# Kernel optimization log

Hardware: AMD Instinct MI355X
Metric: run time of the kernel (lower is better)

The kernel has to match this reference:

```python
import jax, jax.numpy as jnp
import numpy as np

HIDDEN = 1024
HEADS = 16
HEAD_DIM = HIDDEN // HEADS  # 64
LOCAL = (128, 128)
ROPE_MAX_POS = LOCAL[0] + LOCAL[1]  # 256 (local attention branch)
ROPE_BASE = 10000.0


def make_rope_cache(max_len, dim, base):
    positions = jnp.arange(max_len, dtype=jnp.float32)
    theta = 1.0 / base ** (jnp.arange(0, dim, 2, dtype=jnp.float32) / dim)
    angles = jnp.einsum('i,j->ij', positions, theta)
    return jnp.stack([jnp.cos(angles), jnp.sin(angles)], axis=-1)  # (max_len, dim//2, 2)


def apply_rope(x, cache):
    # x: (B, S, H, D); cache: (max_pos, D//2, 2)
    S = x.shape[1]
    pos = jnp.arange(S) % cache.shape[0]
    rc = cache[pos][None, :, None, :, :]  # (1, S, 1, D//2, 2)
    xr = x.reshape(*x.shape[:-1], -1, 2)
    x0, x1 = xr[..., 0], xr[..., 1]
    c, s = rc[..., 0], rc[..., 1]
    out = jnp.stack([x0 * c - x1 * s, x1 * c + x0 * s], axis=-1)
    return out.reshape(x.shape)


def sliding_window_mask(S, window, dtype):
    rel = jnp.arange(S)[:, None] - jnp.arange(S)[None, :]
    inside = (rel >= -window[0]) & (rel <= window[1])
    return jnp.where(inside, jnp.zeros((), dtype), -jnp.inf)[None, None]  # (1,1,S,S)


def setup_inputs() -> dict:
    key = jax.random.key(0)
    k1, k2, k3, k4, k5 = jax.random.split(key, 5)
    B, S = 2, 2048
    hidden_states = jax.random.normal(k1, (B, S, HIDDEN), dtype=jnp.float32)
    Wqkv_kernel = jax.random.normal(k2, (HIDDEN, 3 * HIDDEN), dtype=jnp.float32) / np.sqrt(HIDDEN)
    Wqkv_bias = jnp.zeros((3 * HIDDEN,), dtype=jnp.float32)
    Wo_kernel = jax.random.normal(k3, (HIDDEN, HIDDEN), dtype=jnp.float32) / np.sqrt(HIDDEN)
    Wo_bias = jnp.zeros((HIDDEN,), dtype=jnp.float32)
    rope_cache = make_rope_cache(ROPE_MAX_POS, HEAD_DIM, ROPE_BASE)
    return {
        'hidden_states': hidden_states,
        'Wqkv_kernel': Wqkv_kernel,
        'Wqkv_bias': Wqkv_bias,
        'Wo_kernel': Wo_kernel,
        'Wo_bias': Wo_bias,
        'rope_cache': rope_cache,
    }


def reference(hidden_states, Wqkv_kernel, Wqkv_bias, Wo_kernel, Wo_bias, rope_cache):
    B, S, _ = hidden_states.shape
    qkv = hidden_states @ Wqkv_kernel + Wqkv_bias  # (B,S,3*HIDDEN)
    qkv = qkv.reshape(B, S, 3, HEADS, HEAD_DIM)
    q = qkv[:, :, 0]  # (B,S,H,D)
    k = qkv[:, :, 1]
    v = qkv[:, :, 2]
    q = apply_rope(q, rope_cache)
    k = apply_rope(k, rope_cache)
    # to (B,H,S,D)
    q = jnp.transpose(q, (0, 2, 1, 3))
    k = jnp.transpose(k, (0, 2, 1, 3))
    v = jnp.transpose(v, (0, 2, 1, 3))
    scale = jnp.sqrt(jnp.float32(HEAD_DIM))
    scores = jnp.einsum('bhqd,bhkd->bhqk', q, k) / scale
    mask = sliding_window_mask(S, LOCAL, scores.dtype)
    probs = jax.nn.softmax(scores + mask, axis=-1)
    out = jnp.einsum('bhqk,bhkd->bqhd', probs, v).reshape(B, S, HIDDEN)
    out = out @ Wo_kernel + Wo_bias
    return out
```

## Files before the change

### kernel.cpp

```cpp
#include <hip/hip_runtime.h>
#include <hip/hip_bf16.h>

typedef __bf16 bf16x8 __attribute__((ext_vector_type(8)));
typedef __bf16 bf16x4 __attribute__((ext_vector_type(4)));
typedef float f32x4 __attribute__((ext_vector_type(4)));

#define SLEN 2048
#define NHEADS 16
#define HDIM 64

__global__ __launch_bounds__(256) void prep(const float* __restrict__ hidden,
                                            const float* __restrict__ Wqkv,
                                            const float* __restrict__ Wo,
                                            __bf16* __restrict__ A1,
                                            __bf16* __restrict__ Wt,
                                            __bf16* __restrict__ Wot) {
    int b = blockIdx.x;
    if (b < 4096) {
        int i = b * 256 + threadIdx.x;
        float4 v = reinterpret_cast<const float4*>(hidden)[i];
        bf16x4 o = { (__bf16)v.x, (__bf16)v.y, (__bf16)v.z, (__bf16)v.w };
        reinterpret_cast<bf16x4*>(A1)[i] = o;
        return;
    }
    __shared__ float tile[32][33];
    const float* W; __bf16* Dst; int N, n0, kc, bx, wn, j0, JNv;
    if (b < 7168) {
        int bb = b - 4096;
        int bx96 = bb % 96; kc = bb / 96;
        W = Wqkv; Dst = Wt; N = 3072;
        n0 = bx96 * 32;
        bx = bx96 >> 2; wn = (bx96 >> 1) & 1; j0 = (bx96 & 1) * 2; JNv = 4;
    } else {
        int bb = b - 7168;
        int bx32 = bb % 32; kc = bb / 32;
        W = Wo; Dst = Wot; N = 1024;
        n0 = bx32 * 32;
        bx = bx32 >> 1; wn = bx32 & 1; j0 = 0; JNv = 2;
    }
    int k0 = kc * 32;
    int tx = threadIdx.x & 31, ty = threadIdx.x >> 5;
    #pragma unroll
    for (int i = ty; i < 32; i += 8)
        tile[i][tx] = W[(size_t)(k0 + i) * N + n0 + tx];
    __syncthreads();
    if (threadIdx.x < 128) {
        int jh = threadIdx.x >> 6;
        int lane = threadIdx.x & 63;
        int lrow = lane & 15, quad = lane >> 4;
        bf16x8 val;
        #pragma unroll
        for (int i = 0; i < 8; i++)
            val[i] = (__bf16)tile[quad * 8 + i][jh * 16 + lrow];
        size_t idx = ((((size_t)(bx * 32 + kc) * 2 + wn) * JNv + (j0 + jh)) * 64 + lane);
        *reinterpret_cast<bf16x8*>(Dst + idx * 8) = val;
    }
}

template <int TN>
__global__ __launch_bounds__(256) void gemm_bt(const __bf16* __restrict__ A,
                                               const __bf16* __restrict__ Bfrag,
                                               const float* __restrict__ bias,
                                               float* __restrict__ Cf,
                                               __bf16* __restrict__ Cq,
                                               __bf16* __restrict__ Ck,
                                               __bf16* __restrict__ Cv,
                                               int M, int N, int K, int epi) {
    constexpr int JN = TN / 32;
    __shared__ __align__(16) __bf16 As[2][128 * 40];

    int nb = N / TN;
    int bx = blockIdx.x % nb;
    int by = blockIdx.x / nb;
    int row0 = by * 128, col0 = bx * TN;

    int tid = threadIdx.x;
    int wave = tid >> 6, lane = tid & 63;
    int quad = lane >> 4, lrow = lane & 15;
    int wm = wave >> 1, wn = wave & 1;

    int r1 = tid >> 2;
    int kk = (tid & 3) * 8;
    const __bf16* Aptr = A + (size_t)(row0 + r1) * K + kk;

    const __bf16* Bbase = Bfrag + ((size_t)(bx * 32) * 2 + wn) * JN * 512 + (size_t)lane * 8;

    f32x4 acc[4][JN];
    f32x4 zero = {0.f, 0.f, 0.f, 0.f};
    #pragma unroll
    for (int i = 0; i < 4; i++)
        #pragma unroll
        for (int j = 0; j < JN; j++) acc[i][j] = zero;

    int nkc = K >> 5;

    {
        bf16x8 a0 = *reinterpret_cast<const bf16x8*>(Aptr);
        bf16x8 a1 = *reinterpret_cast<const bf16x8*>(Aptr + (size_t)64 * K);
        *reinterpret_cast<bf16x8*>(&As[0][r1 * 40 + kk]) = a0;
        *reinterpret_cast<bf16x8*>(&As[0][(r1 + 64) * 40 + kk]) = a1;
    }
    bf16x8 bR[JN];
    #pragma unroll
    for (int j = 0; j < JN; j++)
        bR[j] = *reinterpret_cast<const bf16x8*>(Bbase + j * 512);
    __syncthreads();

    for (int kc = 0; kc < nkc; kc++) {
        int p = kc & 1;
        bool more = (kc + 1) < nkc;
        bf16x8 aN0, aN1, bN[JN];
        if (more) {
            int k0 = (kc + 1) * 32;
            aN0 = *reinterpret_cast<const bf16x8*>(Aptr + k0);
            aN1 = *reinterpret_cast<const bf16x8*>(Aptr + (size_t)64 * K + k0);
            #pragma unroll
            for (int j = 0; j < JN; j++)
                bN[j] = *reinterpret_cast<const bf16x8*>(Bbase + (size_t)(kc + 1) * JN * 1024 + j * 512);
        }

        bf16x8 af[4];
        #pragma unroll
        for (int i = 0; i < 4; i++)
            af[i] = *reinterpret_cast<const bf16x8*>(&As[p][(wm * 64 + i * 16 + lrow) * 40 + quad * 8]);
        #pragma unroll
        for (int i = 0; i < 4; i++)
            #pragma unroll
            for (int j = 0; j < JN; j++)
                acc[i][j] = __builtin_amdgcn_mfma_f32_16x16x32_bf16(af[i], bR[j], acc[i][j], 0, 0, 0);

        if (more) {
            *reinterpret_cast<bf16x8*>(&As[p ^ 1][r1 * 40 + kk]) = aN0;
            *reinterpret_cast<bf16x8*>(&As[p ^ 1][(r1 + 64) * 40 + kk]) = aN1;
            __syncthreads();
            #pragma unroll
            for (int j = 0; j < JN; j++) bR[j] = bN[j];
        }
    }

    int part = col0 >> 10;
    #pragma unroll
    for (int i = 0; i < 4; i++) {
        int rowb = row0 + wm * 64 + i * 16 + quad * 4;
        #pragma unroll
        for (int j = 0; j < JN; j++) {
            int col = col0 + wn * (TN / 2) + j * 16 + lrow;
            float bsv = bias[col];
            #pragma unroll
            for (int r = 0; r < 4; r++) {
                int row = rowb + r;
                float v = acc[i][j][r] + bsv;
                if (epi == 0) {
                    Cf[(size_t)row * N + col] = v;
                } else {
                    int h = (col >> 6) & 15;
                    int d = col & 63;
                    int b = row >> 11;
                    int s = row & 2047;
                    __bf16* dst = (part == 0) ? Cq : ((part == 1) ? Ck : Cv);
                    dst[((size_t)(b * NHEADS + h) * SLEN + s) * HDIM + d] = (__bf16)v;
                }
            }
        }
    }
}

__device__ __forceinline__ bf16x8 rope8(bf16x8 v, f32x4 a, f32x4 b) {
    bf16x8 o;
    float e, od;
    e = (float)v[0]; od = (float)v[1];
    o[0] = (__bf16)(e * a[0] - od * a[1]); o[1] = (__bf16)(od * a[0] + e * a[1]);
    e = (float)v[2]; od = (float)v[3];
    o[2] = (__bf16)(e * a[2] - od * a[3]); o[3] = (__bf16)(od * a[2] + e * a[3]);
    e = (float)v[4]; od = (float)v[5];
    o[4] = (__bf16)(e * b[0] - od * b[1]); o[5] = (__bf16)(od * b[0] + e * b[1]);
    e = (float)v[6]; od = (float)v[7];
    o[6] = (__bf16)(e * b[2] - od * b[3]); o[7] = (__bf16)(od * b[2] + e * b[3]);
    return o;
}

__global__ __launch_bounds__(256) void rope_kernel(__bf16* __restrict__ Q,
                                                   __bf16* __restrict__ K,
                                                   const float* __restrict__ rope) {
    int idx = blockIdx.x * 256 + threadIdx.x;
    int chunk = idx & 7;
    int s = (idx >> 3) & 2047;
    int bh = idx >> 14;
    size_t off = ((size_t)bh * SLEN + s) * HDIM + chunk * 8;
    int pos = s & 255;
    const float* rp = rope + (size_t)pos * 64 + chunk * 8;
    f32x4 a = *reinterpret_cast<const f32x4*>(rp);
    f32x4 b = *reinterpret_cast<const f32x4*>(rp + 4);
    bf16x8 qv = *reinterpret_cast<bf16x8*>(Q + off);
    *reinterpret_cast<bf16x8*>(Q + off) = rope8(qv, a, b);
    bf16x8 kv = *reinterpret_cast<bf16x8*>(K + off);
    *reinterpret_cast<bf16x8*>(K + off) = rope8(kv, a, b);
}

__global__ __launch_bounds__(256) void attn_kernel(const __bf16* __restrict__ Q,
                                                   const __bf16* __restrict__ K,
                                                   const __bf16* __restrict__ V,
                                                   __bf16* __restrict__ O) {
    __shared__ __align__(16) __bf16 Vt[64][328];
    __shared__ __align__(16) __bf16 Pl[4][16][80];

    int bh = blockIdx.x & 31;
    int qt = blockIdx.x >> 5;
    int q0 = qt * 64;
    int kbase0 = q0 - 128;
    const __bf16* Qbh = Q + (size_t)bh * SLEN * HDIM;
    const __bf16* Kbh = K + (size_t)bh * SLEN * HDIM;
    const __bf16* Vbh = V + (size_t)bh * SLEN * HDIM;

    int tid = threadIdx.x;
    int wave = tid >> 6, lane = tid & 63;
    int quad = lane >> 4, lrow = lane & 15;
    int wq0 = q0 + wave * 16;

    {
        int dchunk = wave * 16;
        #pragma unroll
        for (int k = 0; k < 5; k++) {
            int off = k * 64 + lane;
            int krow = kbase0 + off;
            krow = min(max(krow, 0), SLEN - 1);
            const __bf16* vp = Vbh + (size_t)krow * HDIM + dchunk;
            bf16x8 v0 = *reinterpret_cast<const bf16x8*>(vp);
            bf16x8 v1 = *reinterpret_cast<const bf16x8*>(vp + 8);
            #pragma unroll
            for (int i = 0; i < 8; i++) {
                Vt[dchunk + i][off] = v0[i];
                Vt[dchunk + 8 + i][off] = v1[i];
            }
        }
    }

    bf16x8 qb0 = *reinterpret_cast<const bf16x8*>(Qbh + (size_t)(wq0 + lrow) * HDIM + quad * 8);
    bf16x8 qb1 = *reinterpret_cast<const bf16x8*>(Qbh + (size_t)(wq0 + lrow) * HDIM + 32 + quad * 8);

    __syncthreads();

    f32x4 zero = {0.f, 0.f, 0.f, 0.f};
    f32x4 acc[4], acc_l = zero;
    #pragma unroll
    for (int t = 0; t < 4; t++) acc[t] = zero;

    bf16x8 ones = { (__bf16)1.f, (__bf16)1.f, (__bf16)1.f, (__bf16)1.f,
                    (__bf16)1.f, (__bf16)1.f, (__bf16)1.f, (__bf16)1.f };

    int cbeg = wave >> 1;
    if (q0 < 128) { int e = (128 - q0) >> 5; if (e > cbeg) cbeg = e; }
    int cend = (16 * wave + 271) >> 5;
    { int e = (2175 - q0) >> 5; if (e < cend) cend = e; }

    auto loadK = [&](int c, bf16x8 (&kf)[2][2]) {
        int kb = kbase0 + c * 32;
        #pragma unroll
        for (int sub = 0; sub < 2; sub++) {
            int kr = kb + sub * 16 + lrow;
            int krc = min(max(kr, 0), SLEN - 1);
            const __bf16* kp = Kbh + (size_t)krc * HDIM;
            kf[sub][0] = *reinterpret_cast<const bf16x8*>(kp + quad * 8);
            kf[sub][1] = *reinterpret_cast<const bf16x8*>(kp + 32 + quad * 8);
        }
    };

    auto qkExp = [&](int c, bf16x8 (&kf)[2][2], int slot) {
        int kb = kbase0 + c * 32;
        int q = wq0 + lrow;
        #pragma unroll
        for (int sub = 0; sub < 2; sub++) {
            f32x4 st = __builtin_amdgcn_mfma_f32_16x16x32_bf16(kf[sub][0], qb0, zero, 0, 0, 0);
            st = __builtin_amdgcn_mfma_f32_16x16x32_bf16(kf[sub][1], qb1, st, 0, 0, 0);
            bf16x4 pk;
            #pragma unroll
            for (int r = 0; r < 4; r++) {
                int key = kb + sub * 16 + quad * 4 + r;
                int rel = key - q;
                bool valid = (rel >= -128) && (rel <= 128) && (key >= 0) && (key < SLEN);
                pk[r] = (__bf16)(valid ? __expf(st[r] * 0.125f) : 0.0f);
            }
            *reinterpret_cast<bf16x4*>(&Pl[wave][lrow][slot * 40 + sub * 16 + quad * 4]) = pk;
        }
    };

    auto pv = [&](int c, int slot) {
        int loc = c * 32;
        bf16x8 bp = *reinterpret_cast<const bf16x8*>(&Pl[wave][lrow][slot * 40 + quad * 8]);
        acc_l = __builtin_amdgcn_mfma_f32_16x16x32_bf16(ones, bp, acc_l, 0, 0, 0);
        #pragma unroll
        for (int t = 0; t < 4; t++) {
            bf16x8 va = *reinterpret_cast<const bf16x8*>(&Vt[t * 16 + lrow][loc + quad * 8]);
            acc[t] = __builtin_amdgcn_mfma_f32_16x16x32_bf16(va, bp, acc[t], 0, 0, 0);
        }
    };

    bf16x8 ka0[2][2], ka1[2][2];
    loadK(cbeg, ka0);
    loadK(cbeg + 1, ka1);
    int c = cbeg;
    while (c + 1 <= cend) {
        bf16x8 kn0[2][2], kn1[2][2];
        loadK(c + 2, kn0);
        loadK(c + 3, kn1);
        qkExp(c, ka0, 0);
        qkExp(c + 1, ka1, 1);
        asm volatile("s_waitcnt lgkmcnt(0)" ::: "memory");
        pv(c, 0);
        pv(c + 1, 1);
        #pragma unroll
        for (int sub = 0; sub < 2; sub++) {
            ka0[sub][0] = kn0[sub][0]; ka0[sub][1] = kn0[sub][1];
            ka1[sub][0] = kn1[sub][0]; ka1[sub][1] = kn1[sub][1];
        }
        c += 2;
    }
    if (c <= cend) {
        qkExp(c, ka0, 0);
        asm volatile("s_waitcnt lgkmcnt(0)" ::: "memory");
        pv(c, 0);
    }

    float inv = 1.0f / acc_l[0];
    int b = bh >> 4, h = bh & 15;
    int q = wq0 + lrow;
    size_t base = ((size_t)b * SLEN + q) * 1024 + h * HDIM;
    #pragma unroll
    for (int t = 0; t < 4; t++) {
        bf16x4 o;
        #pragma unroll
        for (int r = 0; r < 4; r++) o[r] = (__bf16)(acc[t][r] * inv);
        *reinterpret_cast<bf16x4*>(&O[base + t * 16 + quad * 4]) = o;
    }
}

extern "C" void kernel_launch(void* const* d_in, const int* in_sizes, int n_in,
                              void* d_out, int out_size, void* d_ws, size_t ws_size,
                              hipStream_t stream) {
    const float* hidden = (const float*)d_in[0];
    const float* Wqkv   = (const float*)d_in[1];
    const float* bqkv   = (const float*)d_in[2];
    const float* Wo     = (const float*)d_in[3];
    const float* bo     = (const float*)d_in[4];
    const float* rope   = (const float*)d_in[5];
    float* out = (float*)d_out;

    char* ws = (char*)d_ws;
    __bf16* A1  = (__bf16*)(ws);
    __bf16* Wt  = (__bf16*)(ws + 8388608);
    __bf16* Wot = (__bf16*)(ws + 14680064);
    __bf16* Qb  = (__bf16*)(ws + 16777216);
    __bf16* Kb  = (__bf16*)(ws + 25165824);
    __bf16* Vb  = (__bf16*)(ws + 33554432);
    __bf16* AO  = (__bf16*)(ws + 41943040);

    prep<<<8192, 256, 0, stream>>>(hidden, Wqkv, Wo, A1, Wt, Wot);

    gemm_bt<128><<<32 * 24, 256, 0, stream>>>(A1, Wt, bqkv, nullptr, Qb, Kb, Vb,
                                              4096, 3072, 1024, 1);
    rope_kernel<<<2048, 256, 0, stream>>>(Qb, Kb, rope);
    attn_kernel<<<1024, 256, 0, stream>>>(Qb, Kb, Vb, AO);
    gemm_bt<64><<<32 * 16, 256, 0, stream>>>(AO, Wot, bo, out, nullptr, nullptr, nullptr,
                                             4096, 1024, 1024, 0);
}
```

Before: 178.3 us.

## Store V transposed from QKV GEMM epilogue to vectorize attention V staging

The QKV GEMM epilogue now writes the V part in a (B,H,D,S) transposed layout, using 4-element bf16 vector stores along the sequence. The attention kernel then loads V rows with contiguous 16-byte reads straight into shared memory, replacing scattered per-element transposing stores. This cuts LDS bank conflicts and scalar shared-memory writes in attention. The cost is strided stores across rows in the GEMM epilogue, and edge clamping now happens in 8-key groups, which relies on kbase0 being aligned to 8.

```diff
diff --git a/kernel.cpp b/kernel.cpp
--- a/kernel.cpp
+++ b/kernel.cpp
@@ -146,19 +146,25 @@
         for (int j = 0; j < JN; j++) {
             int col = col0 + wn * (TN / 2) + j * 16 + lrow;
             float bsv = bias[col];
-            #pragma unroll
-            for (int r = 0; r < 4; r++) {
-                int row = rowb + r;
-                float v = acc[i][j][r] + bsv;
-                if (epi == 0) {
-                    Cf[(size_t)row * N + col] = v;
+            if (epi == 0) {
+                #pragma unroll
+                for (int r = 0; r < 4; r++)
+                    Cf[(size_t)(rowb + r) * N + col] = acc[i][j][r] + bsv;
+            } else {
+                int h = (col >> 6) & 15;
+                int d = col & 63;
+                int b = rowb >> 11;
+                int s0 = rowb & 2047;
+                if (part == 2) {
+                    bf16x4 vv;
+                    #pragma unroll
+                    for (int r = 0; r < 4; r++) vv[r] = (__bf16)(acc[i][j][r] + bsv);
+                    *reinterpret_cast<bf16x4*>(Cv + ((size_t)(b * NHEADS + h) * HDIM + d) * SLEN + s0) = vv;
                 } else {
-                    int h = (col >> 6) & 15;
-                    int d = col & 63;
-                    int b = row >> 11;
-                    int s = row & 2047;
-                    __bf16* dst = (part == 0) ? Cq : ((part == 1) ? Ck : Cv);
-                    dst[((size_t)(b * NHEADS + h) * SLEN + s) * HDIM + d] = (__bf16)v;
+                    __bf16* dst = (part == 0) ? Cq : Ck;
+                    #pragma unroll
+                    for (int r = 0; r < 4; r++)
+                        dst[((size_t)(b * NHEADS + h) * SLEN + s0 + r) * HDIM + d] = (__bf16)(acc[i][j][r] + bsv);
                 }
             }
         }
@@ -218,20 +224,16 @@
     int wq0 = q0 + wave * 16;
 
     {
-        int dchunk = wave * 16;
-        #pragma unroll
-        for (int k = 0; k < 5; k++) {
-            int off = k * 64 + lane;
-            int krow = kbase0 + off;
-            krow = min(max(krow, 0), SLEN - 1);
-            const __bf16* vp = Vbh + (size_t)krow * HDIM + dchunk;
-            bf16x8 v0 = *reinterpret_cast<const bf16x8*>(vp);
-            bf16x8 v1 = *reinterpret_cast<const bf16x8*>(vp + 8);
-            #pragma unroll
-            for (int i = 0; i < 8; i++) {
-                Vt[dchunk + i][off] = v0[i];
-                Vt[dchunk + 8 + i][off] = v1[i];
-            }
+        int d = tid >> 2;
+        int sub = tid & 3;
+        const __bf16* vrow = Vbh + (size_t)d * SLEN;
+        #pragma unroll
+        for (int g = 0; g < 10; g++) {
+            int off = g * 32 + sub * 8;
+            int key = kbase0 + off;
+            key = min(max(key, 0), SLEN - 8);
+            bf16x8 v = *reinterpret_cast<const bf16x8*>(vrow + key);
+            *reinterpret_cast<bf16x8*>(&Vt[d][off]) = v;
         }
     }
 
```

After: 179.9 us. No clear change (+0.9%).
